# Kernel optimization log

Measured on AMD Instinct MI355X. Metric: run time of the kernel, lower is better.

The kernel has to match this reference:

```python
import jax, jax.numpy as jnp
import numpy as np


def setup_inputs() -> dict:
    key = jax.random.key(0)
    ks = jax.random.split(key, 16)
    B, S, D, H = 32, 2048, 512, 512
    s = 1.0 / np.sqrt(H)
    inp = {
        "x": jax.random.normal(ks[0], (B, H), jnp.float32),
        "context": jax.random.normal(ks[1], (B, S, D), jnp.float32),
        "mask": jnp.zeros((B, S), jnp.bool_),  # False = valid position
        "Wi": jax.random.normal(ks[2], (H, H), jnp.float32) * s,
        "bi": jax.random.normal(ks[3], (H,), jnp.float32) * s,
        "Wc0": jax.random.normal(ks[4], (H, D), jnp.float32) * s,
        "bc0": jax.random.normal(ks[5], (H,), jnp.float32) * s,
        "Wc1": jax.random.normal(ks[6], (H, D), jnp.float32) * s,
        "bc1": jax.random.normal(ks[7], (H,), jnp.float32) * s,
        "Wc2": jax.random.normal(ks[8], (H, D), jnp.float32) * s,
        "bc2": jax.random.normal(ks[9], (H,), jnp.float32) * s,
        "Wc3": jax.random.normal(ks[10], (H, D), jnp.float32) * s,
        "bc3": jax.random.normal(ks[11], (H,), jnp.float32) * s,
        "V": jax.random.uniform(ks[12], (H,), jnp.float32, -s, s),
    }
    return inp


def reference(x, context, mask, Wi, bi, Wc0, bc0, Wc1, bc1, Wc2, bc2, Wc3, bc3, V):
    # mask: True = masked out in the original API; module flips it first.
    valid = ~mask  # [B, S], True = keep

    inp = (x @ Wi.T + bi)[:, :, None]  # [B, H, 1]

    def proj(W, b):
        # Conv1d(D, H, kernel=1) on context.permute(0,2,1) == token-wise GEMM
        return jnp.einsum("bsd,hd->bhs", context, W) + b[None, :, None]  # [B, H, S]

    ctx = jnp.concatenate(
        [proj(Wc0, bc0), proj(Wc1, bc1), proj(Wc2, bc2), proj(Wc3, bc3)], axis=2
    )  # [B, H, 4S]

    t = jnp.tanh(inp + ctx)                      # [B, H, 4S]
    att = jnp.einsum("h,bhs->bs", V, t)          # bmm(V[B,1,H], t).squeeze(1)
    att = 10.0 * jnp.tanh(att)                   # [B, 4S]

    valid4 = jnp.tile(valid, (1, 4))             # mask.repeat(1, 4)
    att = jnp.where(valid4, att, -jnp.inf)
    # torch.no_grad() around the masked fill detaches the rest of the graph
    att = jax.lax.stop_gradient(att)

    ans = jax.nn.softmax(att, axis=1)            # [B, 4S]
    p = jnp.max(ans, axis=1)
    indices = jnp.argmax(ans, axis=1)
    return indices[:, None], p[:, None], mask
```

## Files before the change

kernel.cpp:

```cpp
#include <hip/hip_runtime.h>
#include <math.h>

typedef __bf16 bf16x8 __attribute__((ext_vector_type(8)));
typedef float f32x4 __attribute__((ext_vector_type(4)));
typedef short short8v __attribute__((ext_vector_type(8)));

#define MARGIN 0.01f
#define NCAND 32

#define WAITL  do { asm volatile("s_waitcnt lgkmcnt(0)" ::: "memory"); __builtin_amdgcn_sched_barrier(0); } while (0)
#define WAITV0 do { asm volatile("s_waitcnt vmcnt(0)" ::: "memory"); __builtin_amdgcn_sched_barrier(0); } while (0)
#define WAITV4 do { asm volatile("s_waitcnt vmcnt(4)" ::: "memory"); __builtin_amdgcn_sched_barrier(0); } while (0)
#define WAITV8 do { asm volatile("s_waitcnt vmcnt(8)" ::: "memory"); __builtin_amdgcn_sched_barrier(0); } while (0)
#define RBAR   do { __builtin_amdgcn_sched_barrier(0); __builtin_amdgcn_s_barrier(); } while (0)
#define BARR   __builtin_amdgcn_s_barrier()

#define MFMA_PHASE(NH, B0, B1) do { \
    WAITL; \
    __builtin_amdgcn_s_setprio(1); \
    _Pragma("unroll") \
    for (int mi = 0; mi < 8; ++mi) { \
      acc[mi][2*(NH)]   = __builtin_amdgcn_mfma_f32_16x16x32_bf16(a[mi], (B0), acc[mi][2*(NH)],   0, 0, 0); \
      acc[mi][2*(NH)+1] = __builtin_amdgcn_mfma_f32_16x16x32_bf16(a[mi], (B1), acc[mi][2*(NH)+1], 0, 0, 0); \
    } \
    __builtin_amdgcn_s_setprio(0); \
  } while (0)

__device__ __forceinline__ unsigned short f2bf(float f) {
  unsigned u = __float_as_uint(f);
  u += 0x7fffu + ((u >> 16) & 1u);
  return (unsigned short)(u >> 16);
}
__device__ __forceinline__ float tanh_fast(float x) {
  float e = __builtin_amdgcn_exp2f(x * 2.885390081777927f);
  return 1.f - 2.f * __builtin_amdgcn_rcpf(e + 1.f);
}
__device__ __forceinline__ void gl_lds16(const void* g, void* l) {
  __builtin_amdgcn_global_load_lds(
      (const __attribute__((address_space(1))) unsigned int*)g,
      (__attribute__((address_space(3))) unsigned int*)l, 16, 0, 0);
}

__global__ __launch_bounds__(256) void prep_inp_k(const float* __restrict__ x,
    const float* __restrict__ Wi, const float* __restrict__ bi, float* __restrict__ inp) {
  int gid = blockIdx.x * 256 + threadIdx.x;
  int b = gid >> 9, h = gid & 511;
  const float* xr = x + b * 512;
  const float* wr = Wi + h * 512;
  float acc = bi[h];
  #pragma unroll 4
  for (int k = 0; k < 512; k += 4) {
    float4 xv = *(const float4*)(xr + k);
    float4 wv = *(const float4*)(wr + k);
    acc += xv.x * wv.x + xv.y * wv.y + xv.z * wv.z + xv.w * wv.w;
  }
  inp[gid] = acc;
}

__global__ __launch_bounds__(256) void prep_w_pack_k(const float* __restrict__ w0,
    const float* __restrict__ w1, const float* __restrict__ w2, const float* __restrict__ w3,
    short* __restrict__ Whi) {
  int gid = blockIdx.x * 256 + threadIdx.x;
  if (gid >= 131072) return;
  int c = gid & 3, row = (gid >> 2) & 255, TK = gid >> 10;
  int TN = TK >> 4, KS = TK & 15;
  int n = TN * 256 + row;
  int g = n >> 9, h = n & 511;
  const float* w = (g == 0) ? w0 : (g == 1) ? w1 : (g == 2) ? w2 : w3;
  int csrc = c ^ ((row >> 1) & 3);
  const float* src = w + (size_t)h * 512 + KS * 32 + csrc * 8;
  float f[8];
  *(float4*)&f[0] = *(const float4*)(src);
  *(float4*)&f[4] = *(const float4*)(src + 4);
  short8v hv;
  #pragma unroll
  for (int i = 0; i < 8; ++i) hv[i] = (short)f2bf(f[i]);
  *(short8v*)(Whi + (size_t)gid * 8) = hv;
}

__global__ __launch_bounds__(256) void prep_ctx_pack_k(const float* __restrict__ ctx,
    short* __restrict__ Chi) {
  int gid = blockIdx.x * 256 + threadIdx.x;
  int c = gid & 3, row = (gid >> 2) & 255, TK = gid >> 10;
  int TM = TK >> 4, KS = TK & 15;
  size_t m = (size_t)TM * 256 + row;
  int csrc = c ^ ((row >> 1) & 3);
  int k = KS * 32 + csrc * 8;
  float f[8];
  *(float4*)&f[0] = *(const float4*)(ctx + m * 512 + k);
  *(float4*)&f[4] = *(const float4*)(ctx + m * 512 + k + 4);
  short8v hv;
  #pragma unroll
  for (int i = 0; i < 8; ++i) hv[i] = (short)f2bf(f[i]);
  *(short8v*)(Chi + (size_t)gid * 8) = hv;
}

template<bool PRESPLIT>
__global__ __launch_bounds__(512, 2) void gemm_att_k(
    const float* __restrict__ ctx, const short* __restrict__ Chi,
    const short* __restrict__ Whi,
    const float* __restrict__ inp,
    const float* __restrict__ bc0, const float* __restrict__ bc1,
    const float* __restrict__ bc2, const float* __restrict__ bc3,
    const float* __restrict__ V, float* __restrict__ att) {
  __shared__ __align__(16) short smem[4][2][8192];
  __shared__ float sV[256], sPre[256];

  const int t = threadIdx.x;
  int d = blockIdx.x + (blockIdx.y << 3);
  int work = (d & 7) * 256 + (d >> 3);
  int mt = work >> 3, nt = work & 7;
  int b = mt >> 3;
  int g = nt >> 1, h0 = (nt & 1) * 256;

  if (t < 256) {
    const float* bc = (g == 0) ? bc0 : (g == 1) ? bc1 : (g == 2) ? bc2 : bc3;
    sV[t] = V[h0 + t];
    sPre[t] = inp[b * 512 + h0 + t] + bc[h0 + t];
  }

  const int toff = t * 8;
  auto stageA = [&](int tile) {
    const short* gA = Chi + (((size_t)mt * 16 + tile) << 13) + toff;
    short* lA = &smem[tile & 3][0][0];
    gl_lds16(gA,        lA + toff);
    gl_lds16(gA + 4096, lA + toff + 4096);
  };
  auto stageB = [&](int tile) {
    const short* gB = Whi + (((size_t)nt * 16 + tile) << 13) + toff;
    short* lB = &smem[tile & 3][1][0];
    gl_lds16(gB,        lB + toff);
    gl_lds16(gB + 4096, lB + toff + 4096);
  };
  auto stageA_reg = [&](int tile) {
    #pragma unroll
    for (int pass = 0; pass < 2; ++pass) {
      int cc = pass * 512 + t;
      int c = cc & 3, r = cc >> 2;
      int csrc = c ^ ((r >> 1) & 3);
      int k = tile * 32 + csrc * 8;
      const float* src = ctx + ((size_t)mt * 256 + r) * 512 + k;
      float f[8];
      *(float4*)&f[0] = *(const float4*)src;
      *(float4*)&f[4] = *(const float4*)(src + 4);
      short8v hv;
      #pragma unroll
      for (int i = 0; i < 8; ++i) hv[i] = (short)f2bf(f[i]);
      *(short8v*)(&smem[tile & 3][0][r * 32 + c * 8]) = hv;
    }
  };

  f32x4 acc[8][4];
  #pragma unroll
  for (int i = 0; i < 8; ++i)
    #pragma unroll
    for (int j = 0; j < 4; ++j) acc[i][j] = (f32x4){0.f, 0.f, 0.f, 0.f};

  const int lane = t & 63, wid = t >> 6;
  const int wr = wid >> 2, wc = wid & 3;
  const int fr = lane & 15, fq = lane >> 4;
  const int csw = fq ^ ((fr >> 1) & 3);
  const int abase = (wr * 128 + fr) * 32 + csw * 8;
  const int bbase = (wc * 64 + fr) * 32 + csw * 8;

  if constexpr (PRESPLIT) {
    stageA(0); stageB(0); stageA(1); stageB(1); stageA(2); stageB(2);
    WAITV8;
  } else {
    stageA_reg(0); stageB(0);
    WAITV0;
  }
  BARR;

  #pragma unroll
  for (int tt = 0; tt < 16; ++tt) {
    const short* sa = &smem[tt & 3][0][0];
    const short* sb = &smem[tt & 3][1][0];
    bf16x8 a[8], b0, b1;
    #pragma unroll
    for (int mi = 0; mi < 8; ++mi)
      a[mi] = *(const bf16x8*)(sa + abase + mi * 512);
    b0 = *(const bf16x8*)(sb + bbase);
    b1 = *(const bf16x8*)(sb + bbase + 512);
    if constexpr (PRESPLIT) { if (tt < 13) stageA(tt + 3); }
    else                    { if (tt < 15) stageA_reg(tt + 1); }
    RBAR;
    MFMA_PHASE(0, b0, b1);
    BARR;
    b0 = *(const bf16x8*)(sb + bbase + 1024);
    b1 = *(const bf16x8*)(sb + bbase + 1536);
    if constexpr (PRESPLIT) { if (tt < 13) stageB(tt + 3); }
    else                    { if (tt < 15) stageB(tt + 1); }
    RBAR;
    MFMA_PHASE(1, b0, b1);
    if constexpr (PRESPLIT) {
      if (tt <= 12) { WAITV8; }
      else if (tt == 13) { WAITV4; }
      else if (tt == 14) { WAITV0; }
    } else {
      if (tt < 15) { WAITV0; }
    }
    BARR;
  }

  float vV[4], vP[4];
  #pragma unroll
  for (int ni = 0; ni < 4; ++ni) {
    int j = wc * 64 + ni * 16 + fr;
    vV[ni] = sV[j];
    vP[ni] = sPre[j];
  }
  size_t abatt = (size_t)b * 8192 + (size_t)g * 2048;
  #pragma unroll
  for (int mi = 0; mi < 8; ++mi) {
    #pragma unroll
    for (int r = 0; r < 4; ++r) {
      float sum = 0.f;
      #pragma unroll
      for (int ni = 0; ni < 4; ++ni)
        sum += vV[ni] * tanh_fast(vP[ni] + acc[mi][ni][r]);
      sum += __shfl_xor(sum, 1, 64);
      sum += __shfl_xor(sum, 2, 64);
      sum += __shfl_xor(sum, 4, 64);
      sum += __shfl_xor(sum, 8, 64);
      if (fr == 0) {
        int s = (mt * 256 + wr * 128 + mi * 16 + fq * 4 + r) & 2047;
        atomicAdd(&att[abatt + s], sum);
      }
    }
  }
}

__global__ __launch_bounds__(256) void tail_k(const float* __restrict__ att,
    const unsigned char* __restrict__ mask, const float* __restrict__ ctx,
    const float* __restrict__ Wc0, const float* __restrict__ Wc1,
    const float* __restrict__ Wc2, const float* __restrict__ Wc3,
    const float* __restrict__ bc0, const float* __restrict__ bc1,
    const float* __restrict__ bc2, const float* __restrict__ bc3,
    const float* __restrict__ inp, const float* __restrict__ V,
    float* __restrict__ out) {
  int b = blockIdx.x, t = threadIdx.x;
  __shared__ float sred[256];
  __shared__ float sctx[512];
  __shared__ int scnt;
  __shared__ int scand_j[NCAND];
  __shared__ float scand_a[NCAND];
  __shared__ float sexact[NCAND];

  if (t == 0) scnt = 0;
  float bm = -1e30f;
  for (int j = t; j < 8192; j += 256) {
    if (mask[b * 2048 + (j & 2047)]) continue;
    bm = fmaxf(bm, att[(size_t)b * 8192 + j]);
  }
  sred[t] = bm;
  __syncthreads();
  for (int s2 = 128; s2 > 0; s2 >>= 1) {
    if (t < s2) sred[t] = fmaxf(sred[t], sred[t + s2]);
    __syncthreads();
  }
  float mx = sred[0];
  float Lref = 10.f * tanhf(mx);
  __syncthreads();
  float se = 0.f;
  for (int j = t; j < 8192; j += 256) {
    if (mask[b * 2048 + (j & 2047)]) continue;
    float a = att[(size_t)b * 8192 + j];
    se += expf(10.f * tanhf(a) - Lref);
    if (a >= mx - MARGIN) {
      int slot = atomicAdd(&scnt, 1);
      if (slot < NCAND) { scand_j[slot] = j; scand_a[slot] = a; }
    }
  }
  sred[t] = se;
  __syncthreads();
  for (int s2 = 128; s2 > 0; s2 >>= 1) {
    if (t < s2) sred[t] += sred[t + s2];
    __syncthreads();
  }
  float den = sred[0];
  int n = min(scnt, NCAND);
  for (int j = t; j < 2048; j += 256)
    out[64 + b * 2048 + j] = mask[b * 2048 + j] ? 1.0f : 0.0f;
  for (int i = 0; i < n; ++i) {
    int jj = scand_j[i];
    int g = jj >> 11, s = jj & 2047;
    const float* W  = (g == 0) ? Wc0 : (g == 1) ? Wc1 : (g == 2) ? Wc2 : Wc3;
    const float* bc = (g == 0) ? bc0 : (g == 1) ? bc1 : (g == 2) ? bc2 : bc3;
    const float* cr = ctx + ((size_t)b * 2048 + s) * 512;
    __syncthreads();
    sctx[t] = cr[t];
    sctx[t + 256] = cr[t + 256];
    __syncthreads();
    float total = 0.f;
    #pragma unroll
    for (int hh = 0; hh < 2; ++hh) {
      int h = t + hh * 256;
      const float* wrp = W + (size_t)h * 512;
      float acc = 0.f;
      #pragma unroll 4
      for (int k = 0; k < 512; k += 4) {
        float4 wv = *(const float4*)(wrp + k);
        acc += wv.x * sctx[k] + wv.y * sctx[k + 1] + wv.z * sctx[k + 2] + wv.w * sctx[k + 3];
      }
      total += V[h] * tanhf(inp[b * 512 + h] + bc[h] + acc);
    }
    sred[t] = total;
    __syncthreads();
    for (int s2 = 128; s2 > 0; s2 >>= 1) {
      if (t < s2) sred[t] += sred[t + s2];
      __syncthreads();
    }
    if (t == 0) sexact[i] = sred[0];
  }
  __syncthreads();
  if (t == 0) {
    float dd = den, best = -1e30f;
    int bj = 0x7fffffff;
    for (int i = 0; i < n; ++i) {
      float e = sexact[i];
      int j = scand_j[i];
      dd += expf(10.f * tanhf(e) - Lref) - expf(10.f * tanhf(scand_a[i]) - Lref);
      if (e > best || (e == best && j < bj)) { best = e; bj = j; }
    }
    out[b] = (float)bj;
    out[32 + b] = expf(10.f * tanhf(best) - Lref) / dd;
  }
}

extern "C" void kernel_launch(void* const* d_in, const int* in_sizes, int n_in,
                              void* d_out, int out_size, void* d_ws, size_t ws_size,
                              hipStream_t stream) {
  const float* x    = (const float*)d_in[0];
  const float* ctx  = (const float*)d_in[1];
  const unsigned char* mask = (const unsigned char*)d_in[2];
  const float* Wi   = (const float*)d_in[3];
  const float* bi   = (const float*)d_in[4];
  const float* Wc0  = (const float*)d_in[5];
  const float* bc0  = (const float*)d_in[6];
  const float* Wc1  = (const float*)d_in[7];
  const float* bc1  = (const float*)d_in[8];
  const float* Wc2  = (const float*)d_in[9];
  const float* bc2  = (const float*)d_in[10];
  const float* Wc3  = (const float*)d_in[11];
  const float* bc3  = (const float*)d_in[12];
  const float* V    = (const float*)d_in[13];
  float* out = (float*)d_out;

  float* inp    = (float*)d_ws;
  float* att    = inp + 16384;
  short* Whi    = (short*)(att + 262144);
  short* Chi    = Whi + 1048576;
  size_t need = (size_t)((char*)(Chi + 33554432) - (char*)d_ws);
  bool presplit = ws_size >= need;

  hipMemsetAsync(att, 0, 262144 * sizeof(float), stream);
  prep_inp_k<<<64, 256, 0, stream>>>(x, Wi, bi, inp);
  prep_w_pack_k<<<512, 256, 0, stream>>>(Wc0, Wc1, Wc2, Wc3, Whi);
  if (presplit) {
    prep_ctx_pack_k<<<16384, 256, 0, stream>>>(ctx, Chi);
    gemm_att_k<true><<<dim3(8, 256), 512, 0, stream>>>(ctx, Chi, Whi,
        inp, bc0, bc1, bc2, bc3, V, att);
  } else {
    gemm_att_k<false><<<dim3(8, 256), 512, 0, stream>>>(ctx, nullptr, Whi,
        inp, bc0, bc1, bc2, bc3, V, att);
  }
  tail_k<<<32, 256, 0, stream>>>(att, mask, ctx, Wc0, Wc1, Wc2, Wc3,
      bc0, bc1, bc2, bc3, inp, V, out);
}
```

Before: 322.3 us.

## Restructure GEMM main loop into single phase, drop LDS swizzle, use DPP reduction

Merges the two MFMA phases per K-tile into one phase that reads all four B fragments up front, then issues the next tile's global-to-LDS loads after the MFMAs, with one barrier per iteration instead of three. Removes the XOR swizzle from the packing kernels and LDS reads, which simplifies addressing but may bring back LDS bank conflicts. Partially unrolls the loop by four instead of fully, and replaces the shuffle-xor row reduction with DPP row shifts, writing from lane 15 instead of lane 0. Issuing loads after the compute can reduce the overlap between memory traffic and MFMA work.

```diff
diff --git a/kernel.cpp b/kernel.cpp
--- a/kernel.cpp
+++ b/kernel.cpp
@@ -12,19 +12,7 @@
 #define WAITV0 do { asm volatile("s_waitcnt vmcnt(0)" ::: "memory"); __builtin_amdgcn_sched_barrier(0); } while (0)
 #define WAITV4 do { asm volatile("s_waitcnt vmcnt(4)" ::: "memory"); __builtin_amdgcn_sched_barrier(0); } while (0)
 #define WAITV8 do { asm volatile("s_waitcnt vmcnt(8)" ::: "memory"); __builtin_amdgcn_sched_barrier(0); } while (0)
-#define RBAR   do { __builtin_amdgcn_sched_barrier(0); __builtin_amdgcn_s_barrier(); } while (0)
-#define BARR   __builtin_amdgcn_s_barrier()
-
-#define MFMA_PHASE(NH, B0, B1) do { \
-    WAITL; \
-    __builtin_amdgcn_s_setprio(1); \
-    _Pragma("unroll") \
-    for (int mi = 0; mi < 8; ++mi) { \
-      acc[mi][2*(NH)]   = __builtin_amdgcn_mfma_f32_16x16x32_bf16(a[mi], (B0), acc[mi][2*(NH)],   0, 0, 0); \
-      acc[mi][2*(NH)+1] = __builtin_amdgcn_mfma_f32_16x16x32_bf16(a[mi], (B1), acc[mi][2*(NH)+1], 0, 0, 0); \
-    } \
-    __builtin_amdgcn_s_setprio(0); \
-  } while (0)
+#define BARR   do { __builtin_amdgcn_s_barrier(); __builtin_amdgcn_sched_barrier(0); } while (0)
 
 __device__ __forceinline__ unsigned short f2bf(float f) {
   unsigned u = __float_as_uint(f);
@@ -39,6 +27,18 @@
   __builtin_amdgcn_global_load_lds(
       (const __attribute__((address_space(1))) unsigned int*)g,
       (__attribute__((address_space(3))) unsigned int*)l, 16, 0, 0);
+}
+__device__ __forceinline__ float dpp_row_reduce(float v) {
+  int x;
+  x = __builtin_amdgcn_update_dpp(0, __builtin_bit_cast(int, v), 0x118, 0xf, 0xf, true);
+  v += __builtin_bit_cast(float, x);
+  x = __builtin_amdgcn_update_dpp(0, __builtin_bit_cast(int, v), 0x114, 0xf, 0xf, true);
+  v += __builtin_bit_cast(float, x);
+  x = __builtin_amdgcn_update_dpp(0, __builtin_bit_cast(int, v), 0x112, 0xf, 0xf, true);
+  v += __builtin_bit_cast(float, x);
+  x = __builtin_amdgcn_update_dpp(0, __builtin_bit_cast(int, v), 0x111, 0xf, 0xf, true);
+  v += __builtin_bit_cast(float, x);
+  return v;
 }
 
 __global__ __launch_bounds__(256) void prep_inp_k(const float* __restrict__ x,
@@ -67,8 +67,7 @@
   int n = TN * 256 + row;
   int g = n >> 9, h = n & 511;
   const float* w = (g == 0) ? w0 : (g == 1) ? w1 : (g == 2) ? w2 : w3;
-  int csrc = c ^ ((row >> 1) & 3);
-  const float* src = w + (size_t)h * 512 + KS * 32 + csrc * 8;
+  const float* src = w + (size_t)h * 512 + KS * 32 + c * 8;
   float f[8];
   *(float4*)&f[0] = *(const float4*)(src);
   *(float4*)&f[4] = *(const float4*)(src + 4);
@@ -84,8 +83,7 @@
   int c = gid & 3, row = (gid >> 2) & 255, TK = gid >> 10;
   int TM = TK >> 4, KS = TK & 15;
   size_t m = (size_t)TM * 256 + row;
-  int csrc = c ^ ((row >> 1) & 3);
-  int k = KS * 32 + csrc * 8;
+  int k = KS * 32 + c * 8;
   float f[8];
   *(float4*)&f[0] = *(const float4*)(ctx + m * 512 + k);
   *(float4*)&f[4] = *(const float4*)(ctx + m * 512 + k + 4);
@@ -137,8 +135,7 @@
     for (int pass = 0; pass < 2; ++pass) {
       int cc = pass * 512 + t;
       int c = cc & 3, r = cc >> 2;
-      int csrc = c ^ ((r >> 1) & 3);
-      int k = tile * 32 + csrc * 8;
+      int k = tile * 32 + c * 8;
       const float* src = ctx + ((size_t)mt * 256 + r) * 512 + k;
       float f[8];
       *(float4*)&f[0] = *(const float4*)src;
@@ -159,46 +156,51 @@
   const int lane = t & 63, wid = t >> 6;
   const int wr = wid >> 2, wc = wid & 3;
   const int fr = lane & 15, fq = lane >> 4;
-  const int csw = fq ^ ((fr >> 1) & 3);
-  const int abase = (wr * 128 + fr) * 32 + csw * 8;
-  const int bbase = (wc * 64 + fr) * 32 + csw * 8;
+  const int abase = (wr * 128 + fr) * 32 + fq * 8;
+  const int bbase = (wc * 64 + fr) * 32 + fq * 8;
 
   if constexpr (PRESPLIT) {
     stageA(0); stageB(0); stageA(1); stageB(1); stageA(2); stageB(2);
     WAITV8;
   } else {
     stageA_reg(0); stageB(0);
-    WAITV0;
+    WAITV0; WAITL;
   }
   BARR;
 
-  #pragma unroll
+  #pragma unroll 4
   for (int tt = 0; tt < 16; ++tt) {
     const short* sa = &smem[tt & 3][0][0];
     const short* sb = &smem[tt & 3][1][0];
-    bf16x8 a[8], b0, b1;
+    bf16x8 a[8], b0, b1, b2, b3;
     #pragma unroll
     for (int mi = 0; mi < 8; ++mi)
       a[mi] = *(const bf16x8*)(sa + abase + mi * 512);
     b0 = *(const bf16x8*)(sb + bbase);
     b1 = *(const bf16x8*)(sb + bbase + 512);
-    if constexpr (PRESPLIT) { if (tt < 13) stageA(tt + 3); }
-    else                    { if (tt < 15) stageA_reg(tt + 1); }
-    RBAR;
-    MFMA_PHASE(0, b0, b1);
-    BARR;
-    b0 = *(const bf16x8*)(sb + bbase + 1024);
-    b1 = *(const bf16x8*)(sb + bbase + 1536);
-    if constexpr (PRESPLIT) { if (tt < 13) stageB(tt + 3); }
-    else                    { if (tt < 15) stageB(tt + 1); }
-    RBAR;
-    MFMA_PHASE(1, b0, b1);
+    b2 = *(const bf16x8*)(sb + bbase + 1024);
+    b3 = *(const bf16x8*)(sb + bbase + 1536);
+    WAITL;
+    __builtin_amdgcn_s_setprio(1);
+    #pragma unroll
+    for (int mi = 0; mi < 8; ++mi) {
+      acc[mi][0] = __builtin_amdgcn_mfma_f32_16x16x32_bf16(a[mi], b0, acc[mi][0], 0, 0, 0);
+      acc[mi][1] = __builtin_amdgcn_mfma_f32_16x16x32_bf16(a[mi], b1, acc[mi][1], 0, 0, 0);
+    }
+    #pragma unroll
+    for (int mi = 0; mi < 8; ++mi) {
+      acc[mi][2] = __builtin_amdgcn_mfma_f32_16x16x32_bf16(a[mi], b2, acc[mi][2], 0, 0, 0);
+      acc[mi][3] = __builtin_amdgcn_mfma_f32_16x16x32_bf16(a[mi], b3, acc[mi][3], 0, 0, 0);
+    }
+    __builtin_amdgcn_s_setprio(0);
+    __builtin_amdgcn_sched_barrier(0);
     if constexpr (PRESPLIT) {
-      if (tt <= 12) { WAITV8; }
+      if (tt <= 12) { stageA(tt + 3); stageB(tt + 3); }
+      if (tt <= 12)      { WAITV8; }
       else if (tt == 13) { WAITV4; }
       else if (tt == 14) { WAITV0; }
     } else {
-      if (tt < 15) { WAITV0; }
+      if (tt < 15) { stageA_reg(tt + 1); stageB(tt + 1); WAITV0; WAITL; }
     }
     BARR;
   }
@@ -219,11 +221,8 @@
       #pragma unroll
       for (int ni = 0; ni < 4; ++ni)
         sum += vV[ni] * tanh_fast(vP[ni] + acc[mi][ni][r]);
-      sum += __shfl_xor(sum, 1, 64);
-      sum += __shfl_xor(sum, 2, 64);
-      sum += __shfl_xor(sum, 4, 64);
-      sum += __shfl_xor(sum, 8, 64);
-      if (fr == 0) {
+      sum = dpp_row_reduce(sum);
+      if (fr == 15) {
         int s = (mt * 256 + wr * 128 + mi * 16 + fq * 4 + r) & 2047;
         atomicAdd(&att[abatt + s], sum);
       }
```

Measured after the change: 314.6 us. 2.4% less time.
